# Kernel tuning notes

Hardware: AMD Instinct MI355X
Metric: run time of the kernel (lower is better)

Reference implementation:

```python
import jax, jax.numpy as jnp
import numpy as np

N_TARGETS = 21
R_HW = 7
FM_H, FM_W = 64, 64
N_ROIS = 300


def setup_inputs() -> dict:
    key = jax.random.key(0)
    k1, k2, k3, k4 = jax.random.split(key, 4)
    FM = jax.random.normal(k1, (N_TARGETS * R_HW ** 2, FM_H, FM_W), dtype=jnp.float32)
    # Build valid ROIs (x1, y1, x2, y2) in feature-map pixel coordinates.
    x1 = jax.random.uniform(k2, (N_ROIS,), minval=0.0, maxval=FM_W * 0.6)
    y1 = jax.random.uniform(k3, (N_ROIS,), minval=0.0, maxval=FM_H * 0.6)
    wh = jax.random.uniform(k4, (N_ROIS, 2), minval=R_HW, maxval=FM_W * 0.4)
    x2 = jnp.minimum(x1 + wh[:, 0], FM_W - 1.0)
    y2 = jnp.minimum(y1 + wh[:, 1], FM_H - 1.0)
    rois = jnp.stack([x1, y1, x2, y2], axis=1).astype(jnp.float32)
    return {"FM": FM, "rois": rois, "n_targets": N_TARGETS, "r_hw": R_HW}


def _bin_masks(start, length, r_hw, size, dtype):
    """start, length: [R]; returns [R, r_hw, size] float bin-membership masks."""
    p = jnp.arange(r_hw, dtype=dtype)
    bin_sz = length / r_hw  # [R]
    lo = jnp.floor(start[:, None] + p[None, :] * bin_sz[:, None])          # [R, r_hw]
    hi = jnp.ceil(start[:, None] + (p[None, :] + 1.0) * bin_sz[:, None])   # [R, r_hw]
    lo = jnp.clip(lo, 0.0, size)
    hi = jnp.clip(hi, 0.0, size)
    idx = jnp.arange(size, dtype=dtype)
    mask = (idx[None, None, :] >= lo[:, :, None]) & (idx[None, None, :] < hi[:, :, None])
    return mask.astype(dtype)


def reference(FM, rois, n_targets, r_hw):
    """Position-sensitive ROI pooling (R-FCN).
    FM: [n_targets*r_hw^2, H, W]; rois: [R, 4] as (x1, y1, x2, y2).
    Returns pooled: [R, n_targets, r_hw, r_hw].
    Bin (p, q) of target t averages FM channel t*r_hw^2 + p*r_hw + q over the
    pixels in that bin; empty bins yield 0.
    """
    C, H, W = FM.shape
    dtype = FM.dtype
    FMr = FM.reshape(n_targets, r_hw, r_hw, H, W)  # [t, p, q, h, w]
    x1, y1, x2, y2 = rois[:, 0], rois[:, 1], rois[:, 2], rois[:, 3]
    roi_h = jnp.maximum(y2 - y1, 0.1)
    roi_w = jnp.maximum(x2 - x1, 0.1)
    mask_h = _bin_masks(y1, roi_h, r_hw, H, dtype)  # [R, p, H]
    mask_w = _bin_masks(x1, roi_w, r_hw, W, dtype)  # [R, q, W]
    # Sum over w per output column q, then over h per output row p.
    tmp = jnp.einsum('tpqhw,rqw->rtpqh', FMr, mask_w)
    s = jnp.einsum('rtpqh,rph->rtpq', tmp, mask_h)
    cnt = mask_h.sum(-1)[:, None, :, None] * mask_w.sum(-1)[:, None, None, :]  # [R,1,p,q]
    return s / jnp.maximum(cnt, 1.0)
```

## Files before the change

### kernel.cpp

```cpp
#include <hip/hip_runtime.h>


#define N_TARGETS 21
#define R_HW 7
#define FM_H 64
#define FM_W 64
#define PLANE (FM_H * FM_W)
#define CPT (N_TARGETS * R_HW * R_HW)

__global__ __launch_bounds__(256) void psroi_kernel(
    const float* __restrict__ FM,
    const float* __restrict__ rois,
    float* __restrict__ out,
    int total) {
  int idx = blockIdx.x * blockDim.x + threadIdx.x;
  if (idx >= total) return;

  int c = idx % CPT;
  int r = idx / CPT;
  int q = c % R_HW;
  int p = (c / R_HW) % R_HW;

  const float4 rv = reinterpret_cast<const float4*>(rois)[r];
  float x1 = rv.x, y1 = rv.y, x2 = rv.z, y2 = rv.w;

  float bw = fmaxf(x2 - x1, 0.1f) / (float)R_HW;
  float bh = fmaxf(y2 - y1, 0.1f) / (float)R_HW;

  float lo_wf = fminf(fmaxf(floorf(x1 + (float)q * bw), 0.0f), (float)FM_W);
  float hi_wf = fminf(fmaxf(ceilf (x1 + ((float)q + 1.0f) * bw), 0.0f), (float)FM_W);
  float lo_hf = fminf(fmaxf(floorf(y1 + (float)p * bh), 0.0f), (float)FM_H);
  float hi_hf = fminf(fmaxf(ceilf (y1 + ((float)p + 1.0f) * bh), 0.0f), (float)FM_H);

  int w0 = (int)lo_wf, w1 = (int)hi_wf;
  int h0 = (int)lo_hf, h1 = (int)hi_hf;

  int cnt = max(h1 - h0, 0) * max(w1 - w0, 0);

  int a  = min(w0 & ~3, FM_W - 4);
  int a2 = min(a + 4,   FM_W - 4);

  const float* __restrict__ plane = FM + (size_t)c * PLANE;

  float s = 0.0f;
#pragma unroll
  for (int i = 0; i < 5; ++i) {
    int h  = h0 + i;
    int hc = min(h, FM_H - 1);
    bool hin = (h < h1);
    const float* __restrict__ row = plane + hc * FM_W;
    float4 v0 = *reinterpret_cast<const float4*>(row + a);
    float4 v1 = *reinterpret_cast<const float4*>(row + a2);

    float rs = 0.0f;
    int w;
    w = a + 0;  rs += (w >= w0 && w < w1) ? v0.x : 0.0f;
    w = a + 1;  rs += (w >= w0 && w < w1) ? v0.y : 0.0f;
    w = a + 2;  rs += (w >= w0 && w < w1) ? v0.z : 0.0f;
    w = a + 3;  rs += (w >= w0 && w < w1) ? v0.w : 0.0f;
    w = a + 4;  rs += (w >= w0 && w < w1) ? v1.x : 0.0f;
    w = a + 5;  rs += (w >= w0 && w < w1) ? v1.y : 0.0f;
    w = a + 6;  rs += (w >= w0 && w < w1) ? v1.z : 0.0f;
    w = a + 7;  rs += (w >= w0 && w < w1) ? v1.w : 0.0f;

    s += hin ? rs : 0.0f;
  }

  out[idx] = s / (float)(cnt > 0 ? cnt : 1);
}

extern "C" void kernel_launch(void* const* d_in, const int* in_sizes, int n_in,
                              void* d_out, int out_size, void* d_ws, size_t ws_size,
                              hipStream_t stream) {
  const float* FM   = (const float*)d_in[0];
  const float* rois = (const float*)d_in[1];
  float* out = (float*)d_out;

  int total = out_size;

  int block = 256;
  int grid = (total + block - 1) / block;
  psroi_kernel<<<grid, block, 0, stream>>>(FM, rois, out, total);
}
```

Measured before the change: 83.86 us.

## Stage each feature-map channel plane in LDS and loop ROIs per block

```diff
diff --git a/kernel.cpp b/kernel.cpp
--- a/kernel.cpp
+++ b/kernel.cpp
@@ -12,61 +12,71 @@
     const float* __restrict__ FM,
     const float* __restrict__ rois,
     float* __restrict__ out,
-    int total) {
-  int idx = blockIdx.x * blockDim.x + threadIdx.x;
-  if (idx >= total) return;
+    int n_rois) {
+  __shared__ float sm[PLANE];
 
-  int c = idx % CPT;
-  int r = idx / CPT;
-  int q = c % R_HW;
-  int p = (c / R_HW) % R_HW;
-
-  const float4 rv = reinterpret_cast<const float4*>(rois)[r];
-  float x1 = rv.x, y1 = rv.y, x2 = rv.z, y2 = rv.w;
-
-  float bw = fmaxf(x2 - x1, 0.1f) / (float)R_HW;
-  float bh = fmaxf(y2 - y1, 0.1f) / (float)R_HW;
-
-  float lo_wf = fminf(fmaxf(floorf(x1 + (float)q * bw), 0.0f), (float)FM_W);
-  float hi_wf = fminf(fmaxf(ceilf (x1 + ((float)q + 1.0f) * bw), 0.0f), (float)FM_W);
-  float lo_hf = fminf(fmaxf(floorf(y1 + (float)p * bh), 0.0f), (float)FM_H);
-  float hi_hf = fminf(fmaxf(ceilf (y1 + ((float)p + 1.0f) * bh), 0.0f), (float)FM_H);
-
-  int w0 = (int)lo_wf, w1 = (int)hi_wf;
-  int h0 = (int)lo_hf, h1 = (int)hi_hf;
-
-  int cnt = max(h1 - h0, 0) * max(w1 - w0, 0);
-
-  int a  = min(w0 & ~3, FM_W - 4);
-  int a2 = min(a + 4,   FM_W - 4);
+  const int c   = blockIdx.x;
+  const int tid = threadIdx.x;
 
   const float* __restrict__ plane = FM + (size_t)c * PLANE;
-
-  float s = 0.0f;
 #pragma unroll
-  for (int i = 0; i < 5; ++i) {
-    int h  = h0 + i;
-    int hc = min(h, FM_H - 1);
-    bool hin = (h < h1);
-    const float* __restrict__ row = plane + hc * FM_W;
-    float4 v0 = *reinterpret_cast<const float4*>(row + a);
-    float4 v1 = *reinterpret_cast<const float4*>(row + a2);
-
-    float rs = 0.0f;
-    int w;
-    w = a + 0;  rs += (w >= w0 && w < w1) ? v0.x : 0.0f;
-    w = a + 1;  rs += (w >= w0 && w < w1) ? v0.y : 0.0f;
-    w = a + 2;  rs += (w >= w0 && w < w1) ? v0.z : 0.0f;
-    w = a + 3;  rs += (w >= w0 && w < w1) ? v0.w : 0.0f;
-    w = a + 4;  rs += (w >= w0 && w < w1) ? v1.x : 0.0f;
-    w = a + 5;  rs += (w >= w0 && w < w1) ? v1.y : 0.0f;
-    w = a + 6;  rs += (w >= w0 && w < w1) ? v1.z : 0.0f;
-    w = a + 7;  rs += (w >= w0 && w < w1) ? v1.w : 0.0f;
-
-    s += hin ? rs : 0.0f;
+  for (int i = 0; i < 4; ++i) {
+    int off = (i * 256 + tid) * 4;
+    *reinterpret_cast<float4*>(&sm[off]) =
+        *reinterpret_cast<const float4*>(plane + off);
   }
 
-  out[idx] = s / (float)(cnt > 0 ? cnt : 1);
+  const int pq = c % (R_HW * R_HW);
+  const int p  = pq / R_HW;
+  const int q  = pq % R_HW;
+
+  __syncthreads();
+
+  for (int r = tid; r < n_rois; r += 256) {
+    const float4 rv = reinterpret_cast<const float4*>(rois)[r];
+    const float x1 = rv.x, y1 = rv.y, x2 = rv.z, y2 = rv.w;
+
+    const float bw = fmaxf(x2 - x1, 0.1f) / (float)R_HW;
+    const float bh = fmaxf(y2 - y1, 0.1f) / (float)R_HW;
+
+    float lo_wf = fminf(fmaxf(floorf(x1 + (float)q * bw), 0.0f), (float)FM_W);
+    float hi_wf = fminf(fmaxf(ceilf (x1 + ((float)q + 1.0f) * bw), 0.0f), (float)FM_W);
+    float lo_hf = fminf(fmaxf(floorf(y1 + (float)p * bh), 0.0f), (float)FM_H);
+    float hi_hf = fminf(fmaxf(ceilf (y1 + ((float)p + 1.0f) * bh), 0.0f), (float)FM_H);
+
+    const int w0 = (int)lo_wf, w1 = (int)hi_wf;
+    const int h0 = (int)lo_hf, h1 = (int)hi_hf;
+    const int cnt = max(h1 - h0, 0) * max(w1 - w0, 0);
+
+    const int a  = min(w0 & ~3, FM_W - 4);
+    const int a2 = min(a + 4,   FM_W - 4);
+
+    float s = 0.0f;
+#pragma unroll
+    for (int i = 0; i < 5; ++i) {
+      const int h  = h0 + i;
+      const int hc = min(h, FM_H - 1);
+      const bool hin = (h < h1);
+      const float* __restrict__ row = &sm[hc * FM_W];
+      const float4 v0 = *reinterpret_cast<const float4*>(row + a);
+      const float4 v1 = *reinterpret_cast<const float4*>(row + a2);
+
+      float rs = 0.0f;
+      int w;
+      w = a + 0;  rs += (w >= w0 && w < w1) ? v0.x : 0.0f;
+      w = a + 1;  rs += (w >= w0 && w < w1) ? v0.y : 0.0f;
+      w = a + 2;  rs += (w >= w0 && w < w1) ? v0.z : 0.0f;
+      w = a + 3;  rs += (w >= w0 && w < w1) ? v0.w : 0.0f;
+      w = a + 4;  rs += (w >= w0 && w < w1) ? v1.x : 0.0f;
+      w = a + 5;  rs += (w >= w0 && w < w1) ? v1.y : 0.0f;
+      w = a + 6;  rs += (w >= w0 && w < w1) ? v1.z : 0.0f;
+      w = a + 7;  rs += (w >= w0 && w < w1) ? v1.w : 0.0f;
+
+      s += hin ? rs : 0.0f;
+    }
+
+    out[(size_t)r * CPT + c] = s / (float)(cnt > 0 ? cnt : 1);
+  }
 }
 
 extern "C" void kernel_launch(void* const* d_in, const int* in_sizes, int n_in,
@@ -76,9 +86,7 @@
   const float* rois = (const float*)d_in[1];
   float* out = (float*)d_out;
 
-  int total = out_size;
+  int n_rois = in_sizes[1] / 4;
 
-  int block = 256;
-  int grid = (total + block - 1) / block;
-  psroi_kernel<<<grid, block, 0, stream>>>(FM, rois, out, total);
+  psroi_kernel<<<CPT, 256, 0, stream>>>(FM, rois, out, n_rois);
 }
```

New measurement: 71.49 us. 14.7% less time.
